# Kernel tuning notes

Hardware: AMD Instinct MI355X
Metric: run time of the kernel (lower is better)

The kernel has to match this reference:

```python
import jax, jax.numpy as jnp
import numpy as np

B, N = 4, 1024
DIM, DEPTH, HEADS, DHEAD, MLP = 512, 6, 8, 64, 2048
INNER = HEADS * DHEAD
SCALE = DHEAD ** -0.5
EPS = 1e-5


def setup_inputs() -> dict:
    key = jax.random.key(0)
    ks = jax.random.split(key, 16)
    w = lambda k, shape: (jax.random.normal(k, shape, jnp.float32) * 0.02)
    D = DEPTH
    return {
        "g": jax.random.normal(ks[0], (B, N, DIM), jnp.float32),
        "x": jax.random.normal(ks[1], (B, N, DIM), jnp.float32),
        # PreNorm + SelfAttention
        "ln1_s": jnp.ones((D, DIM)), "ln1_b": jnp.zeros((D, DIM)),
        "Wqkv": w(ks[2], (D, DIM, 3 * INNER)),
        "Wo_sa": w(ks[3], (D, INNER, DIM)), "bo_sa": jnp.zeros((D, DIM)),
        # RelationalCrossAttention
        "lng_s": jnp.ones((D, DIM)), "lng_b": jnp.zeros((D, DIM)),
        "lnx_s": jnp.ones((D, DIM)), "lnx_b": jnp.zeros((D, DIM)),
        "Wq": w(ks[4], (D, DIM, INNER)),
        "Wk": w(ks[5], (D, DIM, INNER)),
        "Wv": w(ks[6], (D, DIM, INNER)), "bv": jnp.zeros((D, INNER)),
        "Wo_ca": w(ks[7], (D, INNER, DIM)), "bo_ca": jnp.zeros((D, DIM)),
        # PreNorm + FeedForward (same module applied twice per layer)
        "lnf_s": jnp.ones((D, DIM)), "lnf_b": jnp.zeros((D, DIM)),
        "W1": w(ks[8], (D, DIM, MLP)), "b1": jnp.zeros((D, MLP)),
        "W2": w(ks[9], (D, MLP, DIM)), "b2": jnp.zeros((D, DIM)),
    }


def _ln(t, s, b):
    m = t.mean(-1, keepdims=True)
    v = ((t - m) ** 2).mean(-1, keepdims=True)
    return (t - m) / jnp.sqrt(v + EPS) * s + b


def _split_heads(t):  # [b, n, h*d] -> [b, h, n, d]
    b, n, _ = t.shape
    return t.reshape(b, n, HEADS, DHEAD).transpose(0, 2, 1, 3)


def _merge_heads(t):  # [b, h, n, d] -> [b, n, h*d]
    b, h, n, d = t.shape
    return t.transpose(0, 2, 1, 3).reshape(b, n, h * d)


def _attend(q, k, v):
    dots = jnp.einsum('bhnd,bhmd->bhnm', q, k) * SCALE
    attn = jax.nn.softmax(jnp.nan_to_num(dots, nan=-jnp.inf), axis=-1)
    attn = jnp.nan_to_num(attn)  # nan_to_num(0.0) post-softmax as in source
    return jnp.einsum('bhnm,bhmd->bhnd', attn, jnp.nan_to_num(v))


def reference(g, x, ln1_s, ln1_b, Wqkv, Wo_sa, bo_sa, lng_s, lng_b, lnx_s, lnx_b,
              Wq, Wk, Wv, bv, Wo_ca, bo_ca, lnf_s, lnf_b, W1, b1, W2, b2):
    for i in range(DEPTH):
        def ff(t):
            h = jax.nn.gelu(_ln(t, lnf_s[i], lnf_b[i]) @ W1[i] + b1[i], approximate=False)
            return h @ W2[i] + b2[i]
        # relational cross attention: q,k from g, v from x
        gn = _ln(g, lng_s[i], lng_b[i])
        xn = _ln(x, lnx_s[i], lnx_b[i])
        q = _split_heads(gn @ Wq[i])
        k = _split_heads(gn @ Wk[i])
        v = _split_heads(xn @ Wv[i] + bv[i])
        x = _merge_heads(_attend(q, k, v)) @ Wo_ca[i] + bo_ca[i] + x
        x = ff(x) + x
        # pre-norm self attention (skip connection enabled)
        sn = _ln(x, ln1_s[i], ln1_b[i])
        qkv = sn @ Wqkv[i]
        qs, ks_, vs = jnp.split(qkv, 3, axis=-1)
        sa = _merge_heads(_attend(_split_heads(qs), _split_heads(ks_), _split_heads(vs)))
        x = sa @ Wo_sa[i] + bo_sa[i] + x
        x = ff(x) + x
    return x
```

## Files before the change

### kernel.cpp

```cpp
#include <hip/hip_runtime.h>
#include <hip/hip_bf16.h>
#include <cstdint>
#include <cstddef>

#define DEV __device__ __forceinline__

using f32x4 = __attribute__((ext_vector_type(4))) float;
using bfx8  = __attribute__((ext_vector_type(8))) __bf16;
using s16x8 = __attribute__((ext_vector_type(8))) short;

DEV uint16_t f2bf(float f) {
    union { float f; uint32_t u; } x; x.f = f;
    uint32_t r = x.u + 0x7fffu + ((x.u >> 16) & 1u);
    return (uint16_t)(r >> 16);
}

DEV float gelu_exact(float v) {
    return 0.5f * v * (1.0f + erff(v * 0.70710678118654752f));
}

DEV f32x4 mfma16(s16x8 a, s16x8 b, f32x4 c) {
    return __builtin_amdgcn_mfma_f32_16x16x32_bf16(
        __builtin_bit_cast(bfx8, a), __builtin_bit_cast(bfx8, b), c, 0, 0, 0);
}

DEV void async_lds16(const void* g, void* l) {
    __builtin_amdgcn_global_load_lds(
        (const __attribute__((address_space(1))) uint32_t*)g,
        (__attribute__((address_space(3))) uint32_t*)l, 16, 0, 0);
}

template<int HAS_SB>
__global__ __launch_bounds__(256)
void ln_t(const float* __restrict__ in, const float* __restrict__ sc,
          const float* __restrict__ bi, uint16_t* __restrict__ out)
{
    const int lane = threadIdx.x & 63;
    const size_t row = (size_t)blockIdx.x * 4 + (threadIdx.x >> 6);
    const float* p = in + row * 512 + lane * 8;
    float4 a = *(const float4*)p;
    float4 b4 = *(const float4*)(p + 4);
    float v[8] = {a.x, a.y, a.z, a.w, b4.x, b4.y, b4.z, b4.w};
    float s = 0.f, sq = 0.f;
#pragma unroll
    for (int j = 0; j < 8; ++j) { s += v[j]; sq += v[j] * v[j]; }
#pragma unroll
    for (int o = 1; o < 64; o <<= 1) { s += __shfl_xor(s, o); sq += __shfl_xor(sq, o); }
    const float mean = s * (1.0f / 512.0f);
    const float var  = sq * (1.0f / 512.0f) - mean * mean;
    const float rstd = rsqrtf(var + 1e-5f);
    const int c = lane * 8;
    uint16_t o8[8];
#pragma unroll
    for (int j = 0; j < 8; ++j) {
        float z = (v[j] - mean) * rstd;
        if (HAS_SB) z = z * sc[c + j] + bi[c + j];
        o8[j] = f2bf(z);
    }
    uint4 pk;
    pk.x = (uint32_t)o8[0] | ((uint32_t)o8[1] << 16);
    pk.y = (uint32_t)o8[2] | ((uint32_t)o8[3] << 16);
    pk.z = (uint32_t)o8[4] | ((uint32_t)o8[5] << 16);
    pk.w = (uint32_t)o8[6] | ((uint32_t)o8[7] << 16);
    *reinterpret_cast<uint4*>(out + row * 512 + c) = pk;
}

__global__ __launch_bounds__(256)
void wtrans(const float* __restrict__ W, uint16_t* __restrict__ WT, int K, int N,
            size_t lstride, int row0, const float* __restrict__ kscale)
{
    __shared__ float tile[32][33];
    const int l = blockIdx.z;
    const int k0 = blockIdx.x * 32, n0 = blockIdx.y * 32;
    const float* Wl = W + (size_t)l * K * N;
    uint16_t* WTl = WT + (size_t)l * lstride;
    const int tx = threadIdx.x, ty = threadIdx.y;
#pragma unroll
    for (int j = 0; j < 4; ++j) {
        const int k = k0 + ty + j * 8;
        float w = Wl[(size_t)k * N + n0 + tx];
        if (kscale) w *= kscale[l * K + k];
        tile[ty + j * 8][tx] = w;
    }
    __syncthreads();
#pragma unroll
    for (int j = 0; j < 4; ++j)
        WTl[(size_t)(row0 + n0 + ty + j * 8) * K + k0 + tx] = f2bf(tile[tx][ty + j * 8]);
}

__global__ __launch_bounds__(256)
void bfold(const float* __restrict__ b, const float* __restrict__ Wq,
           const float* __restrict__ Wk, float* __restrict__ out)
{
    const int n = blockIdx.x * 256 + threadIdx.x;
    const int l = blockIdx.y, sel = blockIdx.z;
    const float* bb = b + l * 512;
    const float* W = (sel ? Wk : Wq) + (size_t)l * 512 * 512;
    float s = 0.f;
    for (int k = 0; k < 512; ++k) s += bb[k] * W[(size_t)k * 512 + n];
    out[l * 1024 + sel * 512 + n] = s;
}

template<int BM, int BN, int NWR, int NWC, int MINW,
         int HAS_BIAS, int HAS_RESID, int DO_GELU, int OUT_BF16, int OUT_VT, int SPLITK>
__global__ __launch_bounds__(NWR * NWC * 64, MINW)
void gemm10(const uint16_t* __restrict__ A, const uint16_t* __restrict__ BT,
            const float* __restrict__ bias, const float* __restrict__ resid,
            void* __restrict__ outp, uint16_t* __restrict__ vt,
            int M, int N, int K)
{
    constexpr int NT = NWR * NWC * 64;
    constexpr int WM = BM / NWR, WN = BN / NWC;
    constexpr int FM = WM / 16, FN = WN / 16;
    constexpr int ASLOTS = 8 * BM, BSLOTS = 8 * BN, TOT = ASLOTS + BSLOTS;
    constexpr int S = TOT / NT;
    __shared__ uint16_t As[ASLOTS * 8];
    __shared__ uint16_t Bs[BSLOTS * 8];
    const int tid = threadIdx.x, lane = tid & 63;
    const int w = tid >> 6, wr = w / NWC, wc = w % NWC;
    const int kg = lane >> 4, lr = lane & 15;
    const int nbn = N / BN, nbm = M / BM;
    const int rect_m = nbm >> 1, rect_n = nbn >> 2;
    const int xcd = blockIdx.x & 7, c = blockIdx.x >> 3;
    const int bm = (xcd >> 2) * rect_m + c / rect_n;
    const int bn = (xcd & 3) * rect_n + c % rect_n;
    const size_t m0 = (size_t)bm * BM;
    const size_t n0 = (size_t)bn * BN;
    const int kh = K / SPLITK;
    const int kbase = (SPLITK > 1) ? blockIdx.y * kh : 0;

    f32x4 acc[FM][FN] = {};
    for (int k0 = kbase; k0 < kbase + kh; k0 += 64) {
#pragma unroll
        for (int j = 0; j < S; ++j) {
            const int s = j * NT + tid;
            if (s < ASLOTS) {
                const int sub = s / BM, row = s % BM;
                async_lds16(A + (m0 + row) * K + k0 + sub * 8, &As[s * 8]);
            } else {
                const int s2 = s - ASLOTS;
                const int sub = s2 / BN, row = s2 % BN;
                async_lds16(BT + (n0 + row) * K + k0 + sub * 8, &Bs[s2 * 8]);
            }
        }
        __syncthreads();
#pragma unroll
        for (int ks = 0; ks < 2; ++ks) {
            s16x8 af[FM], bf[FN];
#pragma unroll
            for (int i = 0; i < FM; ++i)
                af[i] = *(const s16x8*)&As[((ks * 4 + kg) * BM + wr * WM + i * 16 + lr) * 8];
#pragma unroll
            for (int j = 0; j < FN; ++j)
                bf[j] = *(const s16x8*)&Bs[((ks * 4 + kg) * BN + wc * WN + j * 16 + lr) * 8];
#pragma unroll
            for (int i = 0; i < FM; ++i)
#pragma unroll
                for (int j = 0; j < FN; ++j)
                    acc[i][j] = mfma16(af[i], bf[j], acc[i][j]);
        }
        __syncthreads();
    }
    if (SPLITK > 1) {
        float* pout = (float*)outp + (size_t)blockIdx.y * M * (size_t)N;
#pragma unroll
        for (int i = 0; i < FM; ++i) {
            const size_t rbase = m0 + wr * WM + i * 16 + kg * 4;
#pragma unroll
            for (int j = 0; j < FN; ++j) {
                const size_t col = n0 + wc * WN + j * 16 + lr;
#pragma unroll
                for (int r = 0; r < 4; ++r)
                    pout[(rbase + r) * (size_t)N + col] = acc[i][j][r];
            }
        }
        return;
    }
    if (OUT_VT == 1 || (OUT_VT == 2 && n0 >= 1024)) {
#pragma unroll
        for (int i = 0; i < FM; ++i) {
            const size_t rbase = m0 + wr * WM + i * 16 + kg * 4;
            const int b = (int)(rbase >> 10), nloc = (int)(rbase & 1023);
#pragma unroll
            for (int j = 0; j < FN; ++j) {
                const int col = (int)n0 + wc * WN + j * 16 + lr;
                const int c2 = (OUT_VT == 2) ? col - 1024 : col;
                const float bval = HAS_BIAS ? bias[c2] : 0.0f;
                const int h = c2 >> 6, d = c2 & 63;
                ushort4 pk;
                pk.x = f2bf(acc[i][j][0] + bval);
                pk.y = f2bf(acc[i][j][1] + bval);
                pk.z = f2bf(acc[i][j][2] + bval);
                pk.w = f2bf(acc[i][j][3] + bval);
                *(ushort4*)&vt[((size_t)(b * 8 + h) * 64 + d) * 1024 + nloc] = pk;
            }
        }
        return;
    }
#pragma unroll
    for (int i = 0; i < FM; ++i) {
        const size_t rbase = m0 + wr * WM + i * 16 + kg * 4;
#pragma unroll
        for (int j = 0; j < FN; ++j) {
            const size_t col = n0 + wc * WN + j * 16 + lr;
            const float bval = HAS_BIAS ? bias[col] : 0.0f;
#pragma unroll
            for (int r = 0; r < 4; ++r) {
                const size_t row = rbase + r;
                float v = acc[i][j][r] + bval;
                if (DO_GELU)  v = gelu_exact(v);
                if (HAS_RESID) v += resid[row * (size_t)N + col];
                if (OUT_BF16) ((uint16_t*)outp)[row * (size_t)N + col] = f2bf(v);
                else          ((float*)outp)[row * (size_t)N + col] = v;
            }
        }
    }
}

template<int DO_LN>
__global__ __launch_bounds__(256)
void reduce_ln(const float* __restrict__ p, const float* __restrict__ bias,
               float* __restrict__ x, const float* __restrict__ sc,
               const float* __restrict__ bi, uint16_t* __restrict__ xn)
{
    const int lane = threadIdx.x & 63;
    const size_t row = (size_t)blockIdx.x * 4 + (threadIdx.x >> 6);
    const int c = lane * 8;
    const size_t off = row * 512 + c;
    float v[8];
    {
        float4 r0 = *(const float4*)(x + off), r1 = *(const float4*)(x + off + 4);
        float4 s0 = *(const float4*)(bias + c), s1 = *(const float4*)(bias + c + 4);
        v[0] = r0.x + s0.x; v[1] = r0.y + s0.y; v[2] = r0.z + s0.z; v[3] = r0.w + s0.w;
        v[4] = r1.x + s1.x; v[5] = r1.y + s1.y; v[6] = r1.z + s1.z; v[7] = r1.w + s1.w;
    }
#pragma unroll
    for (int t = 0; t < 4; ++t) {
        const float* pt = p + (size_t)t * 4096 * 512 + off;
        float4 a0 = *(const float4*)pt, a1 = *(const float4*)(pt + 4);
        v[0] += a0.x; v[1] += a0.y; v[2] += a0.z; v[3] += a0.w;
        v[4] += a1.x; v[5] += a1.y; v[6] += a1.z; v[7] += a1.w;
    }
    *(float4*)(x + off)     = make_float4(v[0], v[1], v[2], v[3]);
    *(float4*)(x + off + 4) = make_float4(v[4], v[5], v[6], v[7]);
    if (DO_LN) {
        float s = 0.f, sq = 0.f;
#pragma unroll
        for (int j = 0; j < 8; ++j) { s += v[j]; sq += v[j] * v[j]; }
#pragma unroll
        for (int o = 1; o < 64; o <<= 1) { s += __shfl_xor(s, o); sq += __shfl_xor(sq, o); }
        const float mean = s * (1.0f / 512.0f);
        const float var  = sq * (1.0f / 512.0f) - mean * mean;
        const float rstd = rsqrtf(var + 1e-5f);
        uint16_t o8[8];
#pragma unroll
        for (int j = 0; j < 8; ++j)
            o8[j] = f2bf((v[j] - mean) * rstd * sc[c + j] + bi[c + j]);
        uint4 pk;
        pk.x = (uint32_t)o8[0] | ((uint32_t)o8[1] << 16);
        pk.y = (uint32_t)o8[2] | ((uint32_t)o8[3] << 16);
        pk.z = (uint32_t)o8[4] | ((uint32_t)o8[5] << 16);
        pk.w = (uint32_t)o8[6] | ((uint32_t)o8[7] << 16);
        *reinterpret_cast<uint4*>(xn + off) = pk;
    }
}

__global__ __launch_bounds__(512)
void attn_flash(const uint16_t* __restrict__ Qb, const uint16_t* __restrict__ Kb,
                const uint16_t* __restrict__ Vt, uint16_t* __restrict__ Ob,
                int qstride, int kstride, int qoff, int koff)
{
    __shared__ uint16_t Ks[2][4096];
    __shared__ uint16_t Vs[2][4096];
    __shared__ uint16_t Pb[8][1024];
    const int tid = threadIdx.x, lane = tid & 63, w = tid >> 6;
    const int kg = lane >> 4, lr = lane & 15;
    const int bh = blockIdx.y, b = bh >> 3, h = bh & 7;
    const int q0 = blockIdx.x * 128;
    const float CEXP = 0.125f * 1.44269504f;

    s16x8 aq0, aq1;
    {
        const size_t qrow = (size_t)b * 1024 + q0 + w * 16 + lr;
        const uint16_t* qp = Qb + qrow * qstride + qoff + h * 64 + kg * 8;
        aq0 = *(const s16x8*)qp;
        aq1 = *(const s16x8*)(qp + 32);
    }
    const uint16_t* kbase = Kb + (size_t)b * 1024 * kstride + koff + h * 64;
    const uint16_t* vbase = Vt + (size_t)bh * 65536;

    float l_r[4] = {0.f, 0.f, 0.f, 0.f};
    f32x4 acc[4] = {};

    auto stage = [&](int buf, int kv0) {
        const int s = tid;
        const int sub = s >> 6, row = s & 63;
        async_lds16(kbase + (size_t)(kv0 + row) * kstride + sub * 8, &Ks[buf][s * 8]);
        async_lds16(vbase + (size_t)row * 1024 + kv0 + sub * 8,      &Vs[buf][s * 8]);
    };

    stage(0, 0);
    __syncthreads();
    int cur = 0;
    for (int t = 0; t < 16; ++t) {
        if (t < 15) stage(cur ^ 1, (t + 1) * 64);
        f32x4 s4[4];
        __builtin_amdgcn_s_setprio(1);
#pragma unroll
        for (int ni = 0; ni < 4; ++ni) {
            s16x8 bk0 = *(const s16x8*)&Ks[cur][(kg * 64 + ni * 16 + lr) * 8];
            s16x8 bk1 = *(const s16x8*)&Ks[cur][((4 + kg) * 64 + ni * 16 + lr) * 8];
            f32x4 z = {};
            z = mfma16(aq0, bk0, z);
            z = mfma16(aq1, bk1, z);
            s4[ni] = z;
        }
        __builtin_amdgcn_s_setprio(0);
#pragma unroll
        for (int ni = 0; ni < 4; ++ni) {
            const int slotb = (ni * 2 + (lr >> 3)) * 16 + kg * 4;
#pragma unroll
            for (int r = 0; r < 4; ++r) {
                const float pe = __builtin_amdgcn_exp2f(s4[ni][r] * CEXP);
                l_r[r] += pe;
                Pb[w][(slotb + r) * 8 + (lr & 7)] = f2bf(pe);
            }
        }
        s16x8 ap0 = *(const s16x8*)&Pb[w][(kg * 16 + lr) * 8];
        s16x8 ap1 = *(const s16x8*)&Pb[w][((4 + kg) * 16 + lr) * 8];
        __builtin_amdgcn_s_setprio(1);
#pragma unroll
        for (int ni = 0; ni < 4; ++ni) {
            s16x8 bv0 = *(const s16x8*)&Vs[cur][(kg * 64 + ni * 16 + lr) * 8];
            s16x8 bv1 = *(const s16x8*)&Vs[cur][((4 + kg) * 64 + ni * 16 + lr) * 8];
            acc[ni] = mfma16(ap0, bv0, acc[ni]);
            acc[ni] = mfma16(ap1, bv1, acc[ni]);
        }
        __builtin_amdgcn_s_setprio(0);
        __syncthreads();
        cur ^= 1;
    }
    float linv[4];
#pragma unroll
    for (int r = 0; r < 4; ++r) {
        float l = l_r[r];
        l += __shfl_xor(l, 1); l += __shfl_xor(l, 2);
        l += __shfl_xor(l, 4); l += __shfl_xor(l, 8);
        linv[r] = 1.0f / l;
    }
#pragma unroll
    for (int ni = 0; ni < 4; ++ni)
#pragma unroll
        for (int r = 0; r < 4; ++r) {
            const float v = acc[ni][r] * linv[r];
            const size_t row = (size_t)b * 1024 + q0 + w * 16 + kg * 4 + r;
            Ob[row * 512 + h * 64 + ni * 16 + lr] = f2bf(v);
        }
}

extern "C" void kernel_launch(void* const* d_in, const int* in_sizes, int n_in,
                              void* d_out, int out_size, void* d_ws, size_t ws_size,
                              hipStream_t stream)
{
    (void)in_sizes; (void)n_in; (void)out_size; (void)ws_size;
    const float* g     = (const float*)d_in[0];
    const float* x0    = (const float*)d_in[1];
    const float* ln1_s = (const float*)d_in[2];
    const float* ln1_b = (const float*)d_in[3];
    const float* Wqkv  = (const float*)d_in[4];
    const float* Wo_sa = (const float*)d_in[5];
    const float* bo_sa = (const float*)d_in[6];
    const float* lng_s = (const float*)d_in[7];
    const float* lng_b = (const float*)d_in[8];
    const float* lnx_s = (const float*)d_in[9];
    const float* lnx_b = (const float*)d_in[10];
    const float* Wq    = (const float*)d_in[11];
    const float* Wk    = (const float*)d_in[12];
    const float* Wv    = (const float*)d_in[13];
    const float* bv    = (const float*)d_in[14];
    const float* Wo_ca = (const float*)d_in[15];
    const float* bo_ca = (const float*)d_in[16];
    const float* lnf_s = (const float*)d_in[17];
    const float* lnf_b = (const float*)d_in[18];
    const float* W1    = (const float*)d_in[19];
    const float* b1    = (const float*)d_in[20];
    const float* W2    = (const float*)d_in[21];
    const float* b2    = (const float*)d_in[22];

    float* x = (float*)d_out;

    char* p = (char*)d_ws;
    auto carve = [&](size_t n) { char* r = p; p += (n + 255) & ~(size_t)255; return r; };
    uint16_t* WqkT  = (uint16_t*)carve(6ull * 1024 * 512 * 2);
    uint16_t* WvT   = (uint16_t*)carve(6ull * 512 * 512 * 2);
    uint16_t* WocaT = (uint16_t*)carve(6ull * 512 * 512 * 2);
    uint16_t* WqkvT = (uint16_t*)carve(6ull * 1536 * 512 * 2);
    uint16_t* WosaT = (uint16_t*)carve(6ull * 512 * 512 * 2);
    uint16_t* W1T   = (uint16_t*)carve(6ull * 2048 * 512 * 2);
    uint16_t* W2T   = (uint16_t*)carve(6ull * 512 * 2048 * 2);
    float*    bqk   = (float*)carve(6144ull * 4);
    uint16_t* zg    = (uint16_t*)carve(4096ull * 512 * 2);
    uint16_t* qkall = (uint16_t*)carve(4096ull * 6144 * 2);
    uint16_t* xn    = (uint16_t*)carve(4096ull * 512 * 2);
    uint16_t* qkvu  = (uint16_t*)carve(4096ull * 1536 * 2);
    uint16_t* vt    = (uint16_t*)carve(32ull * 64 * 1024 * 2);
    uint16_t* ab    = (uint16_t*)carve(4096ull * 512 * 2);
    uint16_t* hb    = (uint16_t*)carve(4096ull * 2048 * 2);
    float*    pk4   = (float*)carve(4ull * 4096 * 512 * 4);

    dim3 tb(32, 8);
    wtrans<<<dim3(16, 16, 6), tb, 0, stream>>>(Wq,    WqkT,  512, 512,  1024ull * 512, 0,   lng_s);
    wtrans<<<dim3(16, 16, 6), tb, 0, stream>>>(Wk,    WqkT,  512, 512,  1024ull * 512, 512, lng_s);
    wtrans<<<dim3(16, 16, 6), tb, 0, stream>>>(Wv,    WvT,   512, 512,  512ull * 512, 0, nullptr);
    wtrans<<<dim3(16, 16, 6), tb, 0, stream>>>(Wo_ca, WocaT, 512, 512,  512ull * 512, 0, nullptr);
    wtrans<<<dim3(16, 48, 6), tb, 0, stream>>>(Wqkv,  WqkvT, 512, 1536, 1536ull * 512, 0, nullptr);
    wtrans<<<dim3(16, 16, 6), tb, 0, stream>>>(Wo_sa, WosaT, 512, 512,  512ull * 512, 0, nullptr);
    wtrans<<<dim3(16, 64, 6), tb, 0, stream>>>(W1,    W1T,   512, 2048, 2048ull * 512, 0, nullptr);
    wtrans<<<dim3(64, 16, 6), tb, 0, stream>>>(W2,    W2T,   2048, 512, 2048ull * 512, 0, nullptr);
    bfold<<<dim3(2, 6, 2), 256, 0, stream>>>(lng_b, Wq, Wk, bqk);

    hipMemcpyAsync(x, x0, 4096ull * 512 * 4, hipMemcpyDeviceToDevice, stream);

    ln_t<0><<<1024, 256, 0, stream>>>(g, nullptr, nullptr, zg);
    ln_t<1><<<1024, 256, 0, stream>>>(x, lnx_s, lnx_b, xn);
    gemm10<256, 256, 4, 2, 2, 1, 0, 0, 1, 0, 1><<<384, 512, 0, stream>>>(
        zg, WqkT, bqk, nullptr, qkall, nullptr, 4096, 6144, 512);

    const dim3 ga(8, 32);

    for (int l = 0; l < 6; ++l) {
        const size_t o512 = (size_t)l * 512, oW = (size_t)l * 512 * 512;
        const size_t oW1 = (size_t)l * 2048 * 512, oWqkv = (size_t)l * 1536 * 512;
        const size_t o2048 = (size_t)l * 2048;

        gemm10<128, 64, 2, 2, 4, 1, 0, 0, 0, 1, 1><<<256, 256, 0, stream>>>(
            xn, WvT + oW, bv + o512, nullptr, nullptr, vt, 4096, 512, 512);
        attn_flash<<<ga, 512, 0, stream>>>(qkall, qkall, vt, ab, 6144, 6144,
                                           l * 1024, l * 1024 + 512);
        gemm10<128, 64, 2, 2, 4, 1, 1, 0, 0, 0, 1><<<256, 256, 0, stream>>>(
            ab, WocaT + oW, bo_ca + o512, x, x, nullptr, 4096, 512, 512);

        ln_t<1><<<1024, 256, 0, stream>>>(x, lnf_s + o512, lnf_b + o512, xn);
        gemm10<256, 128, 4, 2, 2, 1, 0, 1, 1, 0, 1><<<256, 512, 0, stream>>>(
            xn, W1T + oW1, b1 + o2048, nullptr, hb, nullptr, 4096, 2048, 512);
        gemm10<256, 128, 4, 2, 2, 0, 0, 0, 0, 0, 4><<<dim3(64, 4), 512, 0, stream>>>(
            hb, W2T + oW1, nullptr, nullptr, pk4, nullptr, 4096, 512, 2048);
        reduce_ln<1><<<1024, 256, 0, stream>>>(pk4, b2 + o512, x,
                                               ln1_s + o512, ln1_b + o512, xn);

        gemm10<256, 128, 4, 2, 2, 0, 0, 0, 1, 2, 1><<<192, 512, 0, stream>>>(
            xn, WqkvT + oWqkv, nullptr, nullptr, qkvu, vt, 4096, 1536, 512);
        attn_flash<<<ga, 512, 0, stream>>>(qkvu, qkvu, vt, ab, 1536, 1536, 0, 512);
        gemm10<128, 64, 2, 2, 4, 1, 1, 0, 0, 0, 1><<<256, 256, 0, stream>>>(
            ab, WosaT + oW, bo_sa + o512, x, x, nullptr, 4096, 512, 512);

        ln_t<1><<<1024, 256, 0, stream>>>(x, lnf_s + o512, lnf_b + o512, xn);
        gemm10<256, 128, 4, 2, 2, 1, 0, 1, 1, 0, 1><<<256, 512, 0, stream>>>(
            xn, W1T + oW1, b1 + o2048, nullptr, hb, nullptr, 4096, 2048, 512);
        gemm10<256, 128, 4, 2, 2, 0, 0, 0, 0, 0, 4><<<dim3(64, 4), 512, 0, stream>>>(
            hb, W2T + oW1, nullptr, nullptr, pk4, nullptr, 4096, 512, 2048);
        if (l < 5)
            reduce_ln<1><<<1024, 256, 0, stream>>>(pk4, b2 + o512, x,
                                                   lnx_s + o512 + 512, lnx_b + o512 + 512, xn);
        else
            reduce_ln<0><<<1024, 256, 0, stream>>>(pk4, b2 + o512, x,
                                                   nullptr, nullptr, nullptr);
    }
}
```

Baseline: 1.752 ms.

## Add multi-stage async-LDS pipelined GEMM for the large projection and FFN matmuls

```diff
diff --git a/kernel.cpp b/kernel.cpp
--- a/kernel.cpp
+++ b/kernel.cpp
@@ -29,6 +29,16 @@
         (const __attribute__((address_space(1))) uint32_t*)g,
         (__attribute__((address_space(3))) uint32_t*)l, 16, 0, 0);
 }
+
+template<int N> DEV void wait_vm() {
+    if constexpr (N == 0)      asm volatile("s_waitcnt vmcnt(0)" ::: "memory");
+    else if constexpr (N == 3) asm volatile("s_waitcnt vmcnt(3)" ::: "memory");
+    else if constexpr (N == 4) asm volatile("s_waitcnt vmcnt(4)" ::: "memory");
+    else if constexpr (N == 6) asm volatile("s_waitcnt vmcnt(6)" ::: "memory");
+    else if constexpr (N == 8) asm volatile("s_waitcnt vmcnt(8)" ::: "memory");
+    else static_assert(N == 0, "add vmcnt literal");
+}
+#define SBAR asm volatile("s_barrier" ::: "memory")
 
 template<int HAS_SB>
 __global__ __launch_bounds__(256)
@@ -101,8 +111,134 @@
     out[l * 1024 + sel * 512 + n] = s;
 }
 
+template<int BM, int BN, int HAS_BIAS, int HAS_RESID, int DO_GELU, int OUT_BF16, int OUT_VT, int SPLITK>
+__global__ __launch_bounds__(512, 2)
+void gemmP(const uint16_t* __restrict__ A, const uint16_t* __restrict__ BT,
+           const float* __restrict__ bias, const float* __restrict__ resid,
+           void* __restrict__ outp, uint16_t* __restrict__ vt,
+           int M, int N, int K)
+{
+    constexpr int NWR = 2, NWC = 4;
+    constexpr int WM = BM / NWR, WN = BN / NWC;
+    constexpr int FM = WM / 16, FN = WN / 16;
+    constexpr int ASLOTS = 4 * BM, BSLOTS = 4 * BN, TOT = ASLOTS + BSLOTS;
+    constexpr int S = TOT / 512;
+    static_assert(TOT % 512 == 0, "slot count");
+    __shared__ uint16_t As[4][ASLOTS * 8];
+    __shared__ uint16_t Bs[4][BSLOTS * 8];
+    const int tid = threadIdx.x, lane = tid & 63;
+    const int w = tid >> 6, wr = w / NWC, wc = w % NWC;
+    const int kg = lane >> 4, lr = lane & 15;
+    const int nbn = N / BN, nbm = M / BM;
+    const int rect_m = nbm >> 1, rect_n = nbn >> 2;
+    const int xcd = blockIdx.x & 7, c = blockIdx.x >> 3;
+    const int bm = (xcd >> 2) * rect_m + c / rect_n;
+    const int bn = (xcd & 3) * rect_n + c % rect_n;
+    const size_t m0 = (size_t)bm * BM;
+    const size_t n0 = (size_t)bn * BN;
+    const int kh = K / SPLITK;
+    const int kbase = (SPLITK > 1) ? blockIdx.y * kh : 0;
+    const int nt = kh / 32;
+
+    auto stage = [&](int buf, int tile) {
+        const int k0 = kbase + tile * 32;
+#pragma unroll
+        for (int j = 0; j < S; ++j) {
+            const int s = j * 512 + tid;
+            if (s < ASLOTS) {
+                const int sub = s / BM, row = s % BM;
+                async_lds16(A + (m0 + row) * K + k0 + sub * 8, &As[buf][s * 8]);
+            } else {
+                const int s2 = s - ASLOTS;
+                const int sub = s2 / BN, row = s2 % BN;
+                async_lds16(BT + (n0 + row) * K + k0 + sub * 8, &Bs[buf][s2 * 8]);
+            }
+        }
+    };
+
+    f32x4 acc[FM][FN] = {};
+    stage(0, 0); stage(1, 1); stage(2, 2);
+    for (int t = 0; t < nt; ++t) {
+        const int gap = nt - 1 - t;
+        if (gap >= 2)      wait_vm<2 * S>();
+        else if (gap == 1) wait_vm<S>();
+        else               wait_vm<0>();
+        SBAR;
+        if (t + 3 < nt) stage((t + 3) & 3, t + 3);
+        const int cur = t & 3;
+        s16x8 af[FM], bf[FN];
+#pragma unroll
+        for (int i = 0; i < FM; ++i)
+            af[i] = *(const s16x8*)&As[cur][(kg * BM + wr * WM + i * 16 + lr) * 8];
+#pragma unroll
+        for (int j = 0; j < FN; ++j)
+            bf[j] = *(const s16x8*)&Bs[cur][(kg * BN + wc * WN + j * 16 + lr) * 8];
+        __builtin_amdgcn_s_setprio(1);
+#pragma unroll
+        for (int i = 0; i < FM; ++i)
+#pragma unroll
+            for (int j = 0; j < FN; ++j)
+                acc[i][j] = mfma16(af[i], bf[j], acc[i][j]);
+        __builtin_amdgcn_s_setprio(0);
+    }
+    if (SPLITK > 1) {
+        float* pout = (float*)outp + (size_t)blockIdx.y * M * (size_t)N;
+#pragma unroll
+        for (int i = 0; i < FM; ++i) {
+            const size_t rbase = m0 + wr * WM + i * 16 + kg * 4;
+#pragma unroll
+            for (int j = 0; j < FN; ++j) {
+                const size_t col = n0 + wc * WN + j * 16 + lr;
+#pragma unroll
+                for (int r = 0; r < 4; ++r)
+                    pout[(rbase + r) * (size_t)N + col] = acc[i][j][r];
+            }
+        }
+        return;
+    }
+    if (OUT_VT == 1 || (OUT_VT == 2 && n0 >= 1024)) {
+#pragma unroll
+        for (int i = 0; i < FM; ++i) {
+            const size_t rbase = m0 + wr * WM + i * 16 + kg * 4;
+            const int b = (int)(rbase >> 10), nloc = (int)(rbase & 1023);
+#pragma unroll
+            for (int j = 0; j < FN; ++j) {
+                const int col = (int)n0 + wc * WN + j * 16 + lr;
+                const int c2 = (OUT_VT == 2) ? col - 1024 : col;
+                const float bval = HAS_BIAS ? bias[c2] : 0.0f;
+                const int h = c2 >> 6, d = c2 & 63;
+                ushort4 pk;
+                pk.x = f2bf(acc[i][j][0] + bval);
+                pk.y = f2bf(acc[i][j][1] + bval);
+                pk.z = f2bf(acc[i][j][2] + bval);
+                pk.w = f2bf(acc[i][j][3] + bval);
+                *(ushort4*)&vt[((size_t)(b * 8 + h) * 64 + d) * 1024 + nloc] = pk;
+            }
+        }
+        return;
+    }
+#pragma unroll
+    for (int i = 0; i < FM; ++i) {
+        const size_t rbase = m0 + wr * WM + i * 16 + kg * 4;
+#pragma unroll
+        for (int j = 0; j < FN; ++j) {
+            const size_t col = n0 + wc * WN + j * 16 + lr;
+            const float bval = HAS_BIAS ? bias[col] : 0.0f;
+#pragma unroll
+            for (int r = 0; r < 4; ++r) {
+                const size_t row = rbase + r;
+                float v = acc[i][j][r] + bval;
+                if (DO_GELU)  v = gelu_exact(v);
+                if (HAS_RESID) v += resid[row * (size_t)N + col];
+                if (OUT_BF16) ((uint16_t*)outp)[row * (size_t)N + col] = f2bf(v);
+                else          ((float*)outp)[row * (size_t)N + col] = v;
+            }
+        }
+    }
+}
+
 template<int BM, int BN, int NWR, int NWC, int MINW,
-         int HAS_BIAS, int HAS_RESID, int DO_GELU, int OUT_BF16, int OUT_VT, int SPLITK>
+         int HAS_BIAS, int HAS_RESID, int DO_GELU, int OUT_BF16, int OUT_VT>
 __global__ __launch_bounds__(NWR * NWC * 64, MINW)
 void gemm10(const uint16_t* __restrict__ A, const uint16_t* __restrict__ BT,
             const float* __restrict__ bias, const float* __restrict__ resid,
@@ -126,11 +262,9 @@
     const int bn = (xcd & 3) * rect_n + c % rect_n;
     const size_t m0 = (size_t)bm * BM;
     const size_t n0 = (size_t)bn * BN;
-    const int kh = K / SPLITK;
-    const int kbase = (SPLITK > 1) ? blockIdx.y * kh : 0;
 
     f32x4 acc[FM][FN] = {};
-    for (int k0 = kbase; k0 < kbase + kh; k0 += 64) {
+    for (int k0 = 0; k0 < K; k0 += 64) {
 #pragma unroll
         for (int j = 0; j < S; ++j) {
             const int s = j * NT + tid;
@@ -160,21 +294,6 @@
                     acc[i][j] = mfma16(af[i], bf[j], acc[i][j]);
         }
         __syncthreads();
-    }
-    if (SPLITK > 1) {
-        float* pout = (float*)outp + (size_t)blockIdx.y * M * (size_t)N;
-#pragma unroll
-        for (int i = 0; i < FM; ++i) {
-            const size_t rbase = m0 + wr * WM + i * 16 + kg * 4;
-#pragma unroll
-            for (int j = 0; j < FN; ++j) {
-                const size_t col = n0 + wc * WN + j * 16 + lr;
-#pragma unroll
-                for (int r = 0; r < 4; ++r)
-                    pout[(rbase + r) * (size_t)N + col] = acc[i][j][r];
-            }
-        }
-        return;
     }
     if (OUT_VT == 1 || (OUT_VT == 2 && n0 >= 1024)) {
 #pragma unroll
@@ -423,7 +542,7 @@
 
     ln_t<0><<<1024, 256, 0, stream>>>(g, nullptr, nullptr, zg);
     ln_t<1><<<1024, 256, 0, stream>>>(x, lnx_s, lnx_b, xn);
-    gemm10<256, 256, 4, 2, 2, 1, 0, 0, 1, 0, 1><<<384, 512, 0, stream>>>(
+    gemmP<256, 256, 1, 0, 0, 1, 0, 1><<<384, 512, 0, stream>>>(
         zg, WqkT, bqk, nullptr, qkall, nullptr, 4096, 6144, 512);
 
     const dim3 ga(8, 32);
@@ -433,31 +552,31 @@
         const size_t oW1 = (size_t)l * 2048 * 512, oWqkv = (size_t)l * 1536 * 512;
         const size_t o2048 = (size_t)l * 2048;
 
-        gemm10<128, 64, 2, 2, 4, 1, 0, 0, 0, 1, 1><<<256, 256, 0, stream>>>(
+        gemm10<128, 64, 2, 2, 4, 1, 0, 0, 0, 1><<<256, 256, 0, stream>>>(
             xn, WvT + oW, bv + o512, nullptr, nullptr, vt, 4096, 512, 512);
         attn_flash<<<ga, 512, 0, stream>>>(qkall, qkall, vt, ab, 6144, 6144,
                                            l * 1024, l * 1024 + 512);
-        gemm10<128, 64, 2, 2, 4, 1, 1, 0, 0, 0, 1><<<256, 256, 0, stream>>>(
+        gemm10<128, 64, 2, 2, 4, 1, 1, 0, 0, 0><<<256, 256, 0, stream>>>(
             ab, WocaT + oW, bo_ca + o512, x, x, nullptr, 4096, 512, 512);
 
         ln_t<1><<<1024, 256, 0, stream>>>(x, lnf_s + o512, lnf_b + o512, xn);
-        gemm10<256, 128, 4, 2, 2, 1, 0, 1, 1, 0, 1><<<256, 512, 0, stream>>>(
+        gemmP<256, 128, 1, 0, 1, 1, 0, 1><<<256, 512, 0, stream>>>(
             xn, W1T + oW1, b1 + o2048, nullptr, hb, nullptr, 4096, 2048, 512);
-        gemm10<256, 128, 4, 2, 2, 0, 0, 0, 0, 0, 4><<<dim3(64, 4), 512, 0, stream>>>(
+        gemmP<256, 128, 0, 0, 0, 0, 0, 4><<<dim3(64, 4), 512, 0, stream>>>(
             hb, W2T + oW1, nullptr, nullptr, pk4, nullptr, 4096, 512, 2048);
         reduce_ln<1><<<1024, 256, 0, stream>>>(pk4, b2 + o512, x,
                                                ln1_s + o512, ln1_b + o512, xn);
 
-        gemm10<256, 128, 4, 2, 2, 0, 0, 0, 1, 2, 1><<<192, 512, 0, stream>>>(
+        gemmP<256, 128, 0, 0, 0, 1, 2, 1><<<192, 512, 0, stream>>>(
             xn, WqkvT + oWqkv, nullptr, nullptr, qkvu, vt, 4096, 1536, 512);
         attn_flash<<<ga, 512, 0, stream>>>(qkvu, qkvu, vt, ab, 1536, 1536, 0, 512);
-        gemm10<128, 64, 2, 2, 4, 1, 1, 0, 0, 0, 1><<<256, 256, 0, stream>>>(
+        gemm10<128, 64, 2, 2, 4, 1, 1, 0, 0, 0><<<256, 256, 0, stream>>>(
             ab, WosaT + oW, bo_sa + o512, x, x, nullptr, 4096, 512, 512);
 
         ln_t<1><<<1024, 256, 0, stream>>>(x, lnf_s + o512, lnf_b + o512, xn);
-        gemm10<256, 128, 4, 2, 2, 1, 0, 1, 1, 0, 1><<<256, 512, 0, stream>>>(
+        gemmP<256, 128, 1, 0, 1, 1, 0, 1><<<256, 512, 0, stream>>>(
             xn, W1T + oW1, b1 + o2048, nullptr, hb, nullptr, 4096, 2048, 512);
-        gemm10<256, 128, 4, 2, 2, 0, 0, 0, 0, 0, 4><<<dim3(64, 4), 512, 0, stream>>>(
+        gemmP<256, 128, 0, 0, 0, 0, 0, 4><<<dim3(64, 4), 512, 0, stream>>>(
             hb, W2T + oW1, nullptr, nullptr, pk4, nullptr, 4096, 512, 2048);
         if (l < 5)
             reduce_ln<1><<<1024, 256, 0, stream>>>(pk4, b2 + o512, x,
```

Result: slower. 1.794 ms (+2.4%).
